# Performance work log

Measured on AMD Instinct MI355X. Metric: run time of the kernel, lower is better.

Reference implementation:

```python
import jax, jax.numpy as jnp
import numpy as np

N = 131072
H = 768

def setup_inputs() -> dict:
    key = jax.random.key(0)
    k1, k2, k3, k4 = jax.random.split(key, 4)
    h_i = jax.random.normal(k1, (N, H), dtype=jnp.float32)
    W_weight = jax.random.normal(k2, (H, H), dtype=jnp.float32) * 0.02
    W_bias = jax.random.normal(k3, (H,), dtype=jnp.float32) * 0.02
    v = jax.random.normal(k4, (1, H), dtype=jnp.float32) * 0.1
    return {"h_i": h_i, "W_weight": W_weight, "W_bias": W_bias, "v": v}

def reference(h_i, W_weight, W_bias, v):
    # u_i = tanh(Linear(h_i)) : [N, H]
    u_i = jnp.tanh(h_i @ W_weight.T + W_bias)
    # scores = v @ u_i.T : [1, N]
    scores = v @ u_i.T
    alpha = jax.nn.softmax(scores, axis=1)  # [1, N]
    # weighted sum over N -> [1, H]
    return alpha @ h_i
```

## Files before the change

kernel.cpp:

```cpp
#include <hip/hip_runtime.h>

#define HDIM 768
#define BM 64
#define NCHUNK 24
#define CHUNK_B 49152
#define A_STRIDE 1552

typedef _Float16 f16x8 __attribute__((ext_vector_type(8)));
typedef _Float16 f16x4 __attribute__((ext_vector_type(4)));
typedef float f32x4 __attribute__((ext_vector_type(4)));

#define LDS_A     0
#define LDS_BB    99328
#define LDS_BIAS  148480
#define LDS_V     151552
#define LDS_SRED  154624
#define LDS_E     158720
#define LDS_TOTAL 158976

#define WS_WT    0
#define WS_Z     1179648
#define WS_PART  1179712
#define WS_PART2 7471168
#define WS_NEED  (WS_PART2 + 49152)

__device__ __forceinline__ float tanh_fast(float z) {
    float e2 = __expf(2.0f * z);
    return 1.0f - 2.0f / (e2 + 1.0f);
}

__device__ __forceinline__ void stage16(const void* g, void* l) {
    __builtin_amdgcn_global_load_lds(
        (const __attribute__((address_space(1))) void*)g,
        (__attribute__((address_space(3))) void*)l, 16, 0, 0);
}

__device__ __forceinline__ f16x8 cvt8(f32x4 x0, f32x4 x1) {
    f16x8 f;
    f[0] = (_Float16)x0[0]; f[1] = (_Float16)x0[1];
    f[2] = (_Float16)x0[2]; f[3] = (_Float16)x0[3];
    f[4] = (_Float16)x1[0]; f[5] = (_Float16)x1[1];
    f[6] = (_Float16)x1[2]; f[7] = (_Float16)x1[3];
    return f;
}

__global__ __launch_bounds__(1024) void prep_kernel(
    const float* __restrict__ W, _Float16* __restrict__ Wt,
    float* __restrict__ Z, float* __restrict__ accbuf) {
    int idx = blockIdx.x * 1024 + threadIdx.x;
    if (idx < 73728) {
        int c  = idx / 96;
        int r  = idx - c * 96;
        int kc = r >> 2;
        int q  = r & 3;
        const float* src = W + c * HDIM + kc * 32 + q * 8;
        f32x4 x0 = *(const f32x4*)src;
        f32x4 x1 = *(const f32x4*)(src + 4);
        f16x8 v = cvt8(x0, x1);
        int qs = q ^ ((c >> 1) & 3);
        *(f16x8*)((char*)Wt + (size_t)kc * CHUNK_B + c * 64 + qs * 16) = v;
    }
    if (idx < HDIM) accbuf[idx] = 0.0f;
    if (idx == 0) *Z = 0.0f;
}

__global__ __launch_bounds__(1024, 4) void score_fused_kernel(
    const float* __restrict__ h, const _Float16* __restrict__ Wt,
    const float* __restrict__ bias, const float* __restrict__ vvec,
    float* __restrict__ part, float* __restrict__ accbuf,
    float* __restrict__ Z, int use_part) {

    extern __shared__ char smem[];
    float* bias_s = (float*)(smem + LDS_BIAS);
    float* v_s    = (float*)(smem + LDS_V);
    float* s_red  = (float*)(smem + LDS_SRED);
    float* e_lds  = (float*)(smem + LDS_E);

    const int tid  = threadIdx.x;
    const int wave = tid >> 6;
    const int lane = tid & 63;
    const int l15  = lane & 15;
    const int lhi  = lane >> 4;
    const int row0 = blockIdx.x * BM;

    if (tid < HDIM) { bias_s[tid] = bias[tid]; v_s[tid] = vvec[tid]; }

    const int quad = lhi ^ ((l15 >> 1) & 3);
    const int boff = (wave * 48 + l15) * 64 + quad * 16;

    #pragma unroll
    for (int s = 0; s < 3; ++s) {
        int idx = wave * 3 + s;
        stage16((const char*)Wt + idx * 1024 + lane * 16, smem + LDS_BB + idx * 1024);
    }
    if (tid < 512) {
        int r = tid >> 3, k4 = tid & 7;
        f32x4 x = *(const f32x4*)(h + (size_t)(row0 + r) * HDIM + k4 * 4);
        f16x4 v;
        v[0] = (_Float16)x[0]; v[1] = (_Float16)x[1];
        v[2] = (_Float16)x[2]; v[3] = (_Float16)x[3];
        *(f16x4*)(smem + LDS_A + r * A_STRIDE + k4 * 8) = v;
    }
    __syncthreads();

    f32x4 acc[4][3];
    #pragma unroll
    for (int rt = 0; rt < 4; ++rt)
        #pragma unroll
        for (int ct = 0; ct < 3; ++ct)
            acc[rt][ct] = (f32x4){0.f, 0.f, 0.f, 0.f};

    for (int kc = 0; kc < NCHUNK; ++kc) {
        const bool has = (kc + 1 < NCHUNK);
        f32x4 pa;
        if (has && tid < 512)
            pa = *(const f32x4*)(h + (size_t)(row0 + (tid >> 3)) * HDIM
                                   + (kc + 1) * 32 + (tid & 7) * 4);

        const char* bb = smem + LDS_BB + boff;
        f16x8 b0 = *(const f16x8*)(bb);
        f16x8 b1 = *(const f16x8*)(bb + 1024);
        f16x8 b2 = *(const f16x8*)(bb + 2048);
        const char* ab = smem + LDS_A + l15 * A_STRIDE + kc * 64 + lhi * 16;
        f16x8 a0 = *(const f16x8*)(ab);
        f16x8 a1 = *(const f16x8*)(ab + 16 * A_STRIDE);
        f16x8 a2 = *(const f16x8*)(ab + 32 * A_STRIDE);
        f16x8 a3 = *(const f16x8*)(ab + 48 * A_STRIDE);
        acc[0][0] = __builtin_amdgcn_mfma_f32_16x16x32_f16(a0, b0, acc[0][0], 0, 0, 0);
        acc[0][1] = __builtin_amdgcn_mfma_f32_16x16x32_f16(a0, b1, acc[0][1], 0, 0, 0);
        acc[0][2] = __builtin_amdgcn_mfma_f32_16x16x32_f16(a0, b2, acc[0][2], 0, 0, 0);
        acc[1][0] = __builtin_amdgcn_mfma_f32_16x16x32_f16(a1, b0, acc[1][0], 0, 0, 0);
        acc[1][1] = __builtin_amdgcn_mfma_f32_16x16x32_f16(a1, b1, acc[1][1], 0, 0, 0);
        acc[1][2] = __builtin_amdgcn_mfma_f32_16x16x32_f16(a1, b2, acc[1][2], 0, 0, 0);
        acc[2][0] = __builtin_amdgcn_mfma_f32_16x16x32_f16(a2, b0, acc[2][0], 0, 0, 0);
        acc[2][1] = __builtin_amdgcn_mfma_f32_16x16x32_f16(a2, b1, acc[2][1], 0, 0, 0);
        acc[2][2] = __builtin_amdgcn_mfma_f32_16x16x32_f16(a2, b2, acc[2][2], 0, 0, 0);
        acc[3][0] = __builtin_amdgcn_mfma_f32_16x16x32_f16(a3, b0, acc[3][0], 0, 0, 0);
        acc[3][1] = __builtin_amdgcn_mfma_f32_16x16x32_f16(a3, b1, acc[3][1], 0, 0, 0);
        acc[3][2] = __builtin_amdgcn_mfma_f32_16x16x32_f16(a3, b2, acc[3][2], 0, 0, 0);

        __syncthreads();

        if (has) {
            const char* g = (const char*)Wt + (size_t)(kc + 1) * CHUNK_B;
            #pragma unroll
            for (int s = 0; s < 3; ++s) {
                int idx = wave * 3 + s;
                stage16(g + idx * 1024 + lane * 16, smem + LDS_BB + idx * 1024);
            }
            if (tid < 512) {
                f16x4 v;
                v[0] = (_Float16)pa[0]; v[1] = (_Float16)pa[1];
                v[2] = (_Float16)pa[2]; v[3] = (_Float16)pa[3];
                *(f16x4*)(smem + LDS_A + (tid >> 3) * A_STRIDE + (kc + 1) * 64
                          + (tid & 7) * 8) = v;
            }
        }
        __syncthreads();
    }

    float pr[4][4];
    #pragma unroll
    for (int rt = 0; rt < 4; ++rt)
        #pragma unroll
        for (int r = 0; r < 4; ++r) pr[rt][r] = 0.f;

    #pragma unroll
    for (int ct = 0; ct < 3; ++ct) {
        int col = wave * 48 + ct * 16 + l15;
        float bj = bias_s[col];
        float vj = v_s[col];
        #pragma unroll
        for (int rt = 0; rt < 4; ++rt)
            #pragma unroll
            for (int r = 0; r < 4; ++r)
                pr[rt][r] = fmaf(vj, tanh_fast(acc[rt][ct][r] + bj), pr[rt][r]);
    }
    #pragma unroll
    for (int rt = 0; rt < 4; ++rt)
        #pragma unroll
        for (int r = 0; r < 4; ++r) {
            float x = pr[rt][r];
            x += __shfl_xor(x, 1);
            x += __shfl_xor(x, 2);
            x += __shfl_xor(x, 4);
            x += __shfl_xor(x, 8);
            if (l15 == 0) s_red[wave * 64 + rt * 16 + lhi * 4 + r] = x;
        }
    __syncthreads();

    if (tid < 64) {
        float s = 0.f;
        #pragma unroll
        for (int w = 0; w < 16; ++w) s += s_red[w * 64 + tid];
        float e = __expf(s);
        e_lds[tid] = e;
        float tot = e;
        tot += __shfl_xor(tot, 1);
        tot += __shfl_xor(tot, 2);
        tot += __shfl_xor(tot, 4);
        tot += __shfl_xor(tot, 8);
        tot += __shfl_xor(tot, 16);
        tot += __shfl_xor(tot, 32);
        if (tid == 0) atomicAdd(Z, tot);
    }
    __syncthreads();

    if (tid < HDIM) {
        const _Float16* A = (const _Float16*)(smem + LDS_A);
        float s = 0.f;
        #pragma unroll 8
        for (int i = 0; i < BM; ++i)
            s += e_lds[i] * (float)A[i * (A_STRIDE / 2) + tid];
        if (use_part) part[(size_t)blockIdx.x * HDIM + tid] = s;
        else          atomicAdd(accbuf + tid, s);
    }
}

__global__ __launch_bounds__(128) void fin1_kernel(
    const float* __restrict__ part, float* __restrict__ part2) {
    const int g  = blockIdx.x / 6;
    const int cb = blockIdx.x % 6;
    const int col = cb * 128 + threadIdx.x;
    float s = 0.f;
    #pragma unroll 8
    for (int p = g * 128; p < (g + 1) * 128; ++p) s += part[(size_t)p * HDIM + col];
    part2[g * HDIM + col] = s;
}

__global__ __launch_bounds__(128) void fin2_kernel(
    const float* __restrict__ src, const float* __restrict__ Z,
    float* __restrict__ out, int ngroups) {
    const int col = blockIdx.x * 128 + threadIdx.x;
    float s = 0.f;
    for (int g = 0; g < ngroups; ++g) s += src[g * HDIM + col];
    out[col] = s / (*Z);
}

extern "C" void kernel_launch(void* const* d_in, const int* in_sizes, int n_in,
                              void* d_out, int out_size, void* d_ws, size_t ws_size,
                              hipStream_t stream) {
    const float* h    = (const float*)d_in[0];
    const float* W    = (const float*)d_in[1];
    const float* bias = (const float*)d_in[2];
    const float* vv   = (const float*)d_in[3];
    float* out = (float*)d_out;

    const int n = in_sizes[0] / HDIM;

    char* ws = (char*)d_ws;
    _Float16* Wt  = (_Float16*)(ws + WS_WT);
    float* Z      = (float*)(ws + WS_Z);
    float* part   = (float*)(ws + WS_PART);
    float* part2  = (float*)(ws + WS_PART2);
    float* accbuf = (float*)(ws + WS_PART);

    const int use_part = (ws_size >= (size_t)WS_NEED) ? 1 : 0;

    hipFuncSetAttribute((const void*)score_fused_kernel,
                        hipFuncAttributeMaxDynamicSharedMemorySize, LDS_TOTAL);

    prep_kernel<<<72, 1024, 0, stream>>>(W, Wt, Z, accbuf);

    score_fused_kernel<<<n / BM, 1024, LDS_TOTAL, stream>>>(
        h, Wt, bias, vv, part, accbuf, Z, use_part);

    if (use_part) {
        fin1_kernel<<<96, 128, 0, stream>>>(part, part2);
        fin2_kernel<<<HDIM / 128, 128, 0, stream>>>(part2, Z, out, 16);
    } else {
        fin2_kernel<<<HDIM / 128, 128, 0, stream>>>(accbuf, Z, out, 1);
    }
}
```

Measured before the change: 328.2 us.

## Pipeline W loads as three rotating LDS slabs with fine-grained waitcnt barriers

Splits each 32-wide K chunk of the transposed weight into three 16 KB column slabs held in a three-slot LDS ring. The next slab is prefetched with stage16 while MFMAs run on the current one. The two full __syncthreads per chunk become three lighter s_barrier points gated by explicit vmcnt/lgkmcnt waits. It also spreads the h staging over all 1024 threads with 2-element loads and remaps the output column ownership to match. The aim is to overlap global-to-LDS traffic with MFMA work, at the cost of more barriers per chunk and correctness that depends on the hand-placed wait counts.

After: 360.5 us. 9.9% more time.

```diff
diff --git a/kernel.cpp b/kernel.cpp
--- a/kernel.cpp
+++ b/kernel.cpp
@@ -3,15 +3,16 @@
 #define HDIM 768
 #define BM 64
 #define NCHUNK 24
-#define CHUNK_B 49152
+#define SLAB_B 16384
 #define A_STRIDE 1552
 
 typedef _Float16 f16x8 __attribute__((ext_vector_type(8)));
-typedef _Float16 f16x4 __attribute__((ext_vector_type(4)));
+typedef _Float16 f16x2 __attribute__((ext_vector_type(2)));
 typedef float f32x4 __attribute__((ext_vector_type(4)));
+typedef float f32x2 __attribute__((ext_vector_type(2)));
 
 #define LDS_A     0
-#define LDS_BB    99328
+#define LDS_B     99328
 #define LDS_BIAS  148480
 #define LDS_V     151552
 #define LDS_SRED  154624
@@ -58,7 +59,7 @@
         f32x4 x1 = *(const f32x4*)(src + 4);
         f16x8 v = cvt8(x0, x1);
         int qs = q ^ ((c >> 1) & 3);
-        *(f16x8*)((char*)Wt + (size_t)kc * CHUNK_B + c * 64 + qs * 16) = v;
+        *(f16x8*)((char*)Wt + (size_t)kc * (3 * SLAB_B) + c * 64 + qs * 16) = v;
     }
     if (idx < HDIM) accbuf[idx] = 0.0f;
     if (idx == 0) *Z = 0.0f;
@@ -86,20 +87,14 @@
     if (tid < HDIM) { bias_s[tid] = bias[tid]; v_s[tid] = vvec[tid]; }
 
     const int quad = lhi ^ ((l15 >> 1) & 3);
-    const int boff = (wave * 48 + l15) * 64 + quad * 16;
-
-    #pragma unroll
-    for (int s = 0; s < 3; ++s) {
-        int idx = wave * 3 + s;
-        stage16((const char*)Wt + idx * 1024 + lane * 16, smem + LDS_BB + idx * 1024);
-    }
-    if (tid < 512) {
-        int r = tid >> 3, k4 = tid & 7;
-        f32x4 x = *(const f32x4*)(h + (size_t)(row0 + r) * HDIM + k4 * 4);
-        f16x4 v;
-        v[0] = (_Float16)x[0]; v[1] = (_Float16)x[1];
-        v[2] = (_Float16)x[2]; v[3] = (_Float16)x[3];
-        *(f16x4*)(smem + LDS_A + r * A_STRIDE + k4 * 8) = v;
+    const int boff = (wave * 16 + l15) * 64 + quad * 16;
+
+    stage16((const char*)Wt + tid * 16,          smem + LDS_B + 0 * SLAB_B + tid * 16);
+    stage16((const char*)Wt + SLAB_B + tid * 16, smem + LDS_B + 1 * SLAB_B + tid * 16);
+    {
+        f32x2 a0 = *(const f32x2*)(h + (size_t)(row0 + (tid >> 4)) * HDIM + (tid & 15) * 2);
+        f16x2 h2; h2[0] = (_Float16)a0[0]; h2[1] = (_Float16)a0[1];
+        *(f16x2*)(smem + LDS_A + (tid >> 4) * A_STRIDE + (tid & 15) * 4) = h2;
     }
     __syncthreads();
 
@@ -110,54 +105,66 @@
         for (int ct = 0; ct < 3; ++ct)
             acc[rt][ct] = (f32x4){0.f, 0.f, 0.f, 0.f};
 
+    #pragma unroll 1
     for (int kc = 0; kc < NCHUNK; ++kc) {
-        const bool has = (kc + 1 < NCHUNK);
-        f32x4 pa;
-        if (has && tid < 512)
-            pa = *(const f32x4*)(h + (size_t)(row0 + (tid >> 3)) * HDIM
-                                   + (kc + 1) * 32 + (tid & 7) * 4);
-
-        const char* bb = smem + LDS_BB + boff;
-        f16x8 b0 = *(const f16x8*)(bb);
-        f16x8 b1 = *(const f16x8*)(bb + 1024);
-        f16x8 b2 = *(const f16x8*)(bb + 2048);
-        const char* ab = smem + LDS_A + l15 * A_STRIDE + kc * 64 + lhi * 16;
-        f16x8 a0 = *(const f16x8*)(ab);
-        f16x8 a1 = *(const f16x8*)(ab + 16 * A_STRIDE);
-        f16x8 a2 = *(const f16x8*)(ab + 32 * A_STRIDE);
-        f16x8 a3 = *(const f16x8*)(ab + 48 * A_STRIDE);
-        acc[0][0] = __builtin_amdgcn_mfma_f32_16x16x32_f16(a0, b0, acc[0][0], 0, 0, 0);
-        acc[0][1] = __builtin_amdgcn_mfma_f32_16x16x32_f16(a0, b1, acc[0][1], 0, 0, 0);
-        acc[0][2] = __builtin_amdgcn_mfma_f32_16x16x32_f16(a0, b2, acc[0][2], 0, 0, 0);
-        acc[1][0] = __builtin_amdgcn_mfma_f32_16x16x32_f16(a1, b0, acc[1][0], 0, 0, 0);
-        acc[1][1] = __builtin_amdgcn_mfma_f32_16x16x32_f16(a1, b1, acc[1][1], 0, 0, 0);
-        acc[1][2] = __builtin_amdgcn_mfma_f32_16x16x32_f16(a1, b2, acc[1][2], 0, 0, 0);
-        acc[2][0] = __builtin_amdgcn_mfma_f32_16x16x32_f16(a2, b0, acc[2][0], 0, 0, 0);
-        acc[2][1] = __builtin_amdgcn_mfma_f32_16x16x32_f16(a2, b1, acc[2][1], 0, 0, 0);
-        acc[2][2] = __builtin_amdgcn_mfma_f32_16x16x32_f16(a2, b2, acc[2][2], 0, 0, 0);
-        acc[3][0] = __builtin_amdgcn_mfma_f32_16x16x32_f16(a3, b0, acc[3][0], 0, 0, 0);
-        acc[3][1] = __builtin_amdgcn_mfma_f32_16x16x32_f16(a3, b1, acc[3][1], 0, 0, 0);
-        acc[3][2] = __builtin_amdgcn_mfma_f32_16x16x32_f16(a3, b2, acc[3][2], 0, 0, 0);
-
-        __syncthreads();
-
-        if (has) {
-            const char* g = (const char*)Wt + (size_t)(kc + 1) * CHUNK_B;
-            #pragma unroll
-            for (int s = 0; s < 3; ++s) {
-                int idx = wave * 3 + s;
-                stage16(g + idx * 1024 + lane * 16, smem + LDS_BB + idx * 1024);
+        f16x8 af0, af1, af2, af3;
+        f32x2 pa;
+        {
+            f16x8 bfr = *(const f16x8*)(smem + LDS_B + 0 * SLAB_B + boff);
+            const char* ab = smem + LDS_A + l15 * A_STRIDE + kc * 64 + lhi * 16;
+            af0 = *(const f16x8*)(ab);
+            af1 = *(const f16x8*)(ab + 16 * A_STRIDE);
+            af2 = *(const f16x8*)(ab + 32 * A_STRIDE);
+            af3 = *(const f16x8*)(ab + 48 * A_STRIDE);
+            stage16((const char*)Wt + (size_t)(3 * kc + 2) * SLAB_B + tid * 16,
+                    smem + LDS_B + 2 * SLAB_B + tid * 16);
+            int ka = (kc + 1 < NCHUNK) ? kc + 1 : kc;
+            pa = *(const f32x2*)(h + (size_t)(row0 + (tid >> 4)) * HDIM + ka * 32 + (tid & 15) * 2);
+            asm volatile("s_waitcnt lgkmcnt(0)" ::: "memory");
+            __builtin_amdgcn_sched_barrier(0);
+            acc[0][0] = __builtin_amdgcn_mfma_f32_16x16x32_f16(af0, bfr, acc[0][0], 0, 0, 0);
+            acc[1][0] = __builtin_amdgcn_mfma_f32_16x16x32_f16(af1, bfr, acc[1][0], 0, 0, 0);
+            acc[2][0] = __builtin_amdgcn_mfma_f32_16x16x32_f16(af2, bfr, acc[2][0], 0, 0, 0);
+            acc[3][0] = __builtin_amdgcn_mfma_f32_16x16x32_f16(af3, bfr, acc[3][0], 0, 0, 0);
+            asm volatile("s_waitcnt vmcnt(1)" ::: "memory");
+            __builtin_amdgcn_s_barrier();
+        }
+        {
+            f16x8 bfr = *(const f16x8*)(smem + LDS_B + 1 * SLAB_B + boff);
+            int sg = 3 * kc + 3; if (sg > 71) sg = 71;
+            stage16((const char*)Wt + (size_t)sg * SLAB_B + tid * 16,
+                    smem + LDS_B + 0 * SLAB_B + tid * 16);
+            asm volatile("s_waitcnt lgkmcnt(0)" ::: "memory");
+            __builtin_amdgcn_sched_barrier(0);
+            acc[0][1] = __builtin_amdgcn_mfma_f32_16x16x32_f16(af0, bfr, acc[0][1], 0, 0, 0);
+            acc[1][1] = __builtin_amdgcn_mfma_f32_16x16x32_f16(af1, bfr, acc[1][1], 0, 0, 0);
+            acc[2][1] = __builtin_amdgcn_mfma_f32_16x16x32_f16(af2, bfr, acc[2][1], 0, 0, 0);
+            acc[3][1] = __builtin_amdgcn_mfma_f32_16x16x32_f16(af3, bfr, acc[3][1], 0, 0, 0);
+            asm volatile("s_waitcnt vmcnt(1)" ::: "memory");
+            __builtin_amdgcn_s_barrier();
+        }
+        {
+            f16x8 bfr = *(const f16x8*)(smem + LDS_B + 2 * SLAB_B + boff);
+            int sg = 3 * kc + 4; if (sg > 71) sg = 71;
+            stage16((const char*)Wt + (size_t)sg * SLAB_B + tid * 16,
+                    smem + LDS_B + 1 * SLAB_B + tid * 16);
+            asm volatile("s_waitcnt lgkmcnt(0)" ::: "memory");
+            __builtin_amdgcn_sched_barrier(0);
+            acc[0][2] = __builtin_amdgcn_mfma_f32_16x16x32_f16(af0, bfr, acc[0][2], 0, 0, 0);
+            acc[1][2] = __builtin_amdgcn_mfma_f32_16x16x32_f16(af1, bfr, acc[1][2], 0, 0, 0);
+            acc[2][2] = __builtin_amdgcn_mfma_f32_16x16x32_f16(af2, bfr, acc[2][2], 0, 0, 0);
+            acc[3][2] = __builtin_amdgcn_mfma_f32_16x16x32_f16(af3, bfr, acc[3][2], 0, 0, 0);
+            if (kc + 1 < NCHUNK) {
+                f16x2 h2; h2[0] = (_Float16)pa[0]; h2[1] = (_Float16)pa[1];
+                *(f16x2*)(smem + LDS_A + (tid >> 4) * A_STRIDE + (kc + 1) * 64
+                          + (tid & 15) * 4) = h2;
             }
-            if (tid < 512) {
-                f16x4 v;
-                v[0] = (_Float16)pa[0]; v[1] = (_Float16)pa[1];
-                v[2] = (_Float16)pa[2]; v[3] = (_Float16)pa[3];
-                *(f16x4*)(smem + LDS_A + (tid >> 3) * A_STRIDE + (kc + 1) * 64
-                          + (tid & 7) * 8) = v;
-            }
-        }
-        __syncthreads();
-    }
+            asm volatile("s_waitcnt lgkmcnt(0)" ::: "memory");
+            asm volatile("s_waitcnt vmcnt(1)" ::: "memory");
+            __builtin_amdgcn_s_barrier();
+        }
+    }
+    __syncthreads();
 
     float pr[4][4];
     #pragma unroll
@@ -167,7 +174,7 @@
 
     #pragma unroll
     for (int ct = 0; ct < 3; ++ct) {
-        int col = wave * 48 + ct * 16 + l15;
+        int col = ct * 256 + wave * 16 + l15;
         float bj = bias_s[col];
         float vj = v_s[col];
         #pragma unroll
```
